# Optimization experiments

Measured on AMD Instinct MI355X. Metric: run time of the kernel, lower is better.

The kernel has to match this reference:

```python
import jax, jax.numpy as jnp
import numpy as np
import math

SIZE = 64
SCALE = math.sqrt(SIZE)
EPS = 1e-12  # torch F.normalize default eps

def l2_normalize(x, axis):
    n = jnp.linalg.norm(x, ord=2, axis=axis, keepdims=True)
    return x / jnp.maximum(n, EPS)

def setup_inputs() -> dict:
    key = jax.random.key(0)
    k1, k2, k3 = jax.random.split(key, 3)
    n, l, s, d, v = 8, 2048, 2048, SIZE, SIZE
    return {
        "query": jax.random.normal(k1, (n, l, d), dtype=jnp.float32),
        "key": jax.random.normal(k2, (n, s, d), dtype=jnp.float32),
        "value": jax.random.normal(k3, (n, s, v), dtype=jnp.float32),
        "mask": jnp.ones((n, l, s), dtype=bool),
    }

def reference(query, key, value, mask):
    # rank-3 query path with normalize=True (cosine attention)
    q = l2_normalize(query, 2)
    k = l2_normalize(key, 2)
    score = jnp.einsum('nlk,nsk->nls', q, k) / SCALE
    score = jnp.where(mask, score, -jnp.inf)
    score = jax.nn.softmax(score, axis=2)  # [n, l, s]
    # equivalent to (score.unsqueeze(3) * value.unsqueeze(1)).sum(2)
    output_value = jnp.einsum('nls,nsv->nlv', score, value)
    return (output_value, score)
```

## Files before the change

### kernel.cpp

```cpp
#include <hip/hip_runtime.h>
#include <hip/hip_bf16.h>
#include <math.h>


typedef __bf16 bf16x8 __attribute__((ext_vector_type(8)));
typedef __bf16 bf16x4 __attribute__((ext_vector_type(4)));
typedef float f32x4 __attribute__((ext_vector_type(4)));

#define NB 8
#define LL 2048
#define SS 2048
#define DD 64

__global__ __launch_bounds__(256) void prep_norm(const float* __restrict__ q,
                                                 const float* __restrict__ k,
                                                 __bf16* __restrict__ Qb,
                                                 __bf16* __restrict__ Kb) {
  int w = threadIdx.x >> 6, lane = threadIdx.x & 63;
  int r = blockIdx.x * 4 + w;
  const float* src;
  __bf16* dst;
  float extra;
  if (r < NB * LL) {
    src = q + (size_t)r * DD;
    dst = Qb + (size_t)r * DD;
    extra = 0.125f;
  } else {
    int rk = r - NB * LL;
    src = k + (size_t)rk * DD;
    dst = Kb + (size_t)rk * DD;
    extra = 1.0f;
  }
  float x = src[lane];
  float ss = x * x;
  ss += __shfl_xor(ss, 1);
  ss += __shfl_xor(ss, 2);
  ss += __shfl_xor(ss, 4);
  ss += __shfl_xor(ss, 8);
  ss += __shfl_xor(ss, 16);
  ss += __shfl_xor(ss, 32);
  float nrm = sqrtf(ss);
  float sc = extra / fmaxf(nrm, 1e-12f);
  dst[lane] = (__bf16)(x * sc);
}

__global__ __launch_bounds__(256) void prep_vt(const float* __restrict__ v,
                                               __bf16* __restrict__ Vt) {
  __shared__ __bf16 tile[64][72];
  int n = blockIdx.y;
  int s0 = blockIdx.x * 64;
  int t = threadIdx.x;
#pragma unroll
  for (int it = 0; it < 4; ++it) {
    int idx = t + it * 256;
    int s = idx >> 4, c = idx & 15;
    float4 f = *(const float4*)(v + ((size_t)(n * SS + s0 + s)) * DD + c * 4);
    tile[s][c * 4 + 0] = (__bf16)f.x;
    tile[s][c * 4 + 1] = (__bf16)f.y;
    tile[s][c * 4 + 2] = (__bf16)f.z;
    tile[s][c * 4 + 3] = (__bf16)f.w;
  }
  __syncthreads();
#pragma unroll
  for (int it = 0; it < 4; ++it) {
    int idx = t + it * 256;
    int vv = idx >> 4, c = idx & 15;
    bf16x4 o;
    o[0] = tile[c * 4 + 0][vv];
    o[1] = tile[c * 4 + 1][vv];
    o[2] = tile[c * 4 + 2][vv];
    o[3] = tile[c * 4 + 3][vv];
    *(bf16x4*)(Vt + ((size_t)(n * DD + vv)) * SS + s0 + c * 4) = o;
  }
}

__global__ __launch_bounds__(512, 4) void attn_main(const __bf16* __restrict__ Qb,
                                                    const __bf16* __restrict__ Kb,
                                                    const __bf16* __restrict__ Vt,
                                                    const int* __restrict__ mask,
                                                    float* __restrict__ out_val,
                                                    float* __restrict__ out_score) {
  __shared__ __bf16 e_lds[2][16][136];
  __shared__ float rs_lds[8][16];
  __shared__ float acc_red[4][16][17];

  const int n = blockIdx.y;
  const int l0 = blockIdx.x * 16;

  const int t = threadIdx.x;
  const int w = t >> 6;
  const int lane = t & 63;
  const int m16 = lane & 15;
  const int quad = lane >> 4;
  const int vg = w & 3;
  const int sh = (w >> 2) * 64;

  const __bf16* qrow = Qb + ((size_t)(n * LL + l0 + m16)) * DD;
  bf16x8 aq0 = *(const bf16x8*)(qrow + quad * 8);
  bf16x8 aq1 = *(const bf16x8*)(qrow + 32 + quad * 8);

  const __bf16* kbase = Kb + (size_t)n * SS * DD;
  const __bf16* vrow = Vt + ((size_t)(n * DD + vg * 16 + m16)) * SS + sh;
  const size_t mrow = ((size_t)(n * LL + l0 + m16)) * SS + w * 16 + quad * 4;
  const int* mptr = mask + mrow;

  f32x4 acc_o = {0.f, 0.f, 0.f, 0.f};
  float rsum = 0.f;
  bf16x4 stash[16];

  int4 mkb[4];
  mkb[0] = *(const int4*)(mptr + 0 * 128);
  mkb[1] = *(const int4*)(mptr + 1 * 128);
  mkb[2] = *(const int4*)(mptr + 2 * 128);
  mkb[3] = *(const int4*)(mptr + 3 * 128);

  bf16x8 kpa0, kpa1, kpb0, kpb1;
  {
    const __bf16* kr = kbase + (size_t)(w * 16 + m16) * DD;
    kpa0 = *(const bf16x8*)(kr + quad * 8);
    kpa1 = *(const bf16x8*)(kr + 32 + quad * 8);
  }

#pragma unroll
  for (int c = 0; c < 16; ++c) {
    const int sc = c * 128;
    bf16x8 bv0 = *(const bf16x8*)(vrow + sc + quad * 8);
    bf16x8 bv1 = *(const bf16x8*)(vrow + sc + 32 + quad * 8);
    const int4 mk = mkb[c & 3];
    if (c + 4 < 16) mkb[c & 3] = *(const int4*)(mptr + (size_t)(c + 4) * 128);
    if (c + 1 < 16) {
      const __bf16* kr = kbase + (size_t)(sc + 128 + w * 16 + m16) * DD;
      if (c & 1) {
        kpa0 = *(const bf16x8*)(kr + quad * 8);
        kpa1 = *(const bf16x8*)(kr + 32 + quad * 8);
      } else {
        kpb0 = *(const bf16x8*)(kr + quad * 8);
        kpb1 = *(const bf16x8*)(kr + 32 + quad * 8);
      }
    }
    const bf16x8 kb0 = (c & 1) ? kpb0 : kpa0;
    const bf16x8 kb1 = (c & 1) ? kpb1 : kpa1;
    f32x4 acc = {0.f, 0.f, 0.f, 0.f};
    acc = __builtin_amdgcn_mfma_f32_16x16x32_bf16(kb0, aq0, acc, 0, 0, 0);
    acc = __builtin_amdgcn_mfma_f32_16x16x32_bf16(kb1, aq1, acc, 0, 0, 0);
    float e0 = mk.x ? __expf(acc[0]) : 0.f;
    float e1 = mk.y ? __expf(acc[1]) : 0.f;
    float e2 = mk.z ? __expf(acc[2]) : 0.f;
    float e3 = mk.w ? __expf(acc[3]) : 0.f;
    rsum += (e0 + e1) + (e2 + e3);
    bf16x4 sv;
    sv[0] = (__bf16)e0;
    sv[1] = (__bf16)e1;
    sv[2] = (__bf16)e2;
    sv[3] = (__bf16)e3;
    stash[c] = sv;
    *(bf16x4*)(&e_lds[c & 1][m16][w * 16 + quad * 4]) = sv;
    asm volatile("s_waitcnt lgkmcnt(0)" ::: "memory");
    __builtin_amdgcn_s_barrier();
    bf16x8 ae0 = *(const bf16x8*)(&e_lds[c & 1][m16][sh + quad * 8]);
    bf16x8 ae1 = *(const bf16x8*)(&e_lds[c & 1][m16][sh + 32 + quad * 8]);
    acc_o = __builtin_amdgcn_mfma_f32_16x16x32_bf16(ae0, bv0, acc_o, 0, 0, 0);
    acc_o = __builtin_amdgcn_mfma_f32_16x16x32_bf16(ae1, bv1, acc_o, 0, 0, 0);
  }

  rsum += __shfl_xor(rsum, 16);
  rsum += __shfl_xor(rsum, 32);
  if (quad == 0) rs_lds[w][m16] = rsum;
  if (w >= 4) {
#pragma unroll
    for (int r = 0; r < 4; ++r) acc_red[vg][quad * 4 + r][m16] = acc_o[r];
  }
  __syncthreads();

  float tot = 0.f;
#pragma unroll
  for (int ww = 0; ww < 8; ++ww) tot += rs_lds[ww][m16];
  const float inv_s = 1.0f / tot;

  if (w < 4) {
#pragma unroll
    for (int r = 0; r < 4; ++r) {
      const int row = quad * 4 + r;
      float tr = 0.f;
#pragma unroll
      for (int ww = 0; ww < 8; ++ww) tr += rs_lds[ww][row];
      const float o = (acc_o[r] + acc_red[vg][row][m16]) / tr;
      out_val[((size_t)(n * LL + l0 + row)) * DD + vg * 16 + m16] = o;
    }
  }

  float* orow = out_score + mrow;
#pragma unroll
  for (int c = 0; c < 16; ++c) {
    float4 o;
    o.x = (float)stash[c][0] * inv_s;
    o.y = (float)stash[c][1] * inv_s;
    o.z = (float)stash[c][2] * inv_s;
    o.w = (float)stash[c][3] * inv_s;
    *(float4*)(orow + (size_t)c * 128) = o;
  }
}

extern "C" void kernel_launch(void* const* d_in, const int* in_sizes, int n_in,
                              void* d_out, int out_size, void* d_ws, size_t ws_size,
                              hipStream_t stream) {
  const float* q = (const float*)d_in[0];
  const float* k = (const float*)d_in[1];
  const float* v = (const float*)d_in[2];
  const int* mask = (const int*)d_in[3];

  float* out_val = (float*)d_out;
  float* out_score = out_val + (size_t)NB * LL * DD;

  __bf16* Qb = (__bf16*)d_ws;
  __bf16* Kb = Qb + (size_t)NB * LL * DD;
  __bf16* Vt = Kb + (size_t)NB * SS * DD;

  prep_norm<<<dim3((NB * LL * 2) / 4), dim3(256), 0, stream>>>(q, k, Qb, Kb);
  prep_vt<<<dim3(SS / 64, NB), dim3(256), 0, stream>>>(v, Vt);
  attn_main<<<dim3(LL / 16, NB), dim3(512), 0, stream>>>(Qb, Kb, Vt, mask, out_val, out_score);
}
```

Baseline: 294.6 us.

## Coalesce mask loads and score stores through LDS staging

Mask reads are re-mapped so each half-wavefront reads one contiguous 512-byte row segment. The mask is packed into byte flags in a double-buffered LDS array that the MFMA-layout lanes then read. Score output is staged through an LDS buffer in groups of four chunks, so each row's float4 stores are fully contiguous instead of scattered 16-byte pieces per lane. This aims to improve global coalescing of the two largest memory streams (the mask read and the score write), at the cost of extra LDS traffic, more shared memory and additional barriers.

```diff
diff --git a/kernel.cpp b/kernel.cpp
--- a/kernel.cpp
+++ b/kernel.cpp
@@ -81,8 +81,11 @@
                                                     float* __restrict__ out_val,
                                                     float* __restrict__ out_score) {
   __shared__ __bf16 e_lds[2][16][136];
+  __shared__ unsigned mb_lds[2][16][33];
   __shared__ float rs_lds[8][16];
   __shared__ float acc_red[4][16][17];
+  __shared__ float inv_row[16];
+  __shared__ __bf16 ep_buf[16][520];
 
   const int n = blockIdx.y;
   const int l0 = blockIdx.x * 16;
@@ -101,18 +104,18 @@
 
   const __bf16* kbase = Kb + (size_t)n * SS * DD;
   const __bf16* vrow = Vt + ((size_t)(n * DD + vg * 16 + m16)) * SS + sh;
-  const size_t mrow = ((size_t)(n * LL + l0 + m16)) * SS + w * 16 + quad * 4;
-  const int* mptr = mask + mrow;
+
+  const int mrow_st = t >> 5;
+  const int mcol_st = (t & 31) * 4;
+  const int* mgbase = mask + ((size_t)(n * LL + l0 + mrow_st)) * SS + mcol_st;
 
   f32x4 acc_o = {0.f, 0.f, 0.f, 0.f};
   float rsum = 0.f;
   bf16x4 stash[16];
 
-  int4 mkb[4];
-  mkb[0] = *(const int4*)(mptr + 0 * 128);
-  mkb[1] = *(const int4*)(mptr + 1 * 128);
-  mkb[2] = *(const int4*)(mptr + 2 * 128);
-  mkb[3] = *(const int4*)(mptr + 3 * 128);
+  int4 mreg[2];
+  mreg[0] = *(const int4*)(mgbase + 0 * 128);
+  mreg[1] = *(const int4*)(mgbase + 1 * 128);
 
   bf16x8 kpa0, kpa1, kpb0, kpb1;
   {
@@ -121,13 +124,19 @@
     kpa1 = *(const bf16x8*)(kr + 32 + quad * 8);
   }
 
+  {
+    const int4 m = mreg[0];
+    mb_lds[0][mrow_st][t & 31] = (unsigned)((m.x != 0) | ((m.y != 0) << 8) |
+                                            ((m.z != 0) << 16) | ((m.w != 0) << 24));
+  }
+  asm volatile("s_waitcnt lgkmcnt(0)" ::: "memory");
+  __builtin_amdgcn_s_barrier();
+
 #pragma unroll
   for (int c = 0; c < 16; ++c) {
     const int sc = c * 128;
     bf16x8 bv0 = *(const bf16x8*)(vrow + sc + quad * 8);
     bf16x8 bv1 = *(const bf16x8*)(vrow + sc + 32 + quad * 8);
-    const int4 mk = mkb[c & 3];
-    if (c + 4 < 16) mkb[c & 3] = *(const int4*)(mptr + (size_t)(c + 4) * 128);
     if (c + 1 < 16) {
       const __bf16* kr = kbase + (size_t)(sc + 128 + w * 16 + m16) * DD;
       if (c & 1) {
@@ -138,15 +147,23 @@
         kpb1 = *(const bf16x8*)(kr + 32 + quad * 8);
       }
     }
+    if (c + 2 < 16) mreg[c & 1] = *(const int4*)(mgbase + (size_t)(c + 2) * 128);
+    if (c + 1 < 16) {
+      const int4 m = mreg[(c + 1) & 1];
+      mb_lds[(c + 1) & 1][mrow_st][t & 31] =
+          (unsigned)((m.x != 0) | ((m.y != 0) << 8) | ((m.z != 0) << 16) |
+                     ((m.w != 0) << 24));
+    }
+    const unsigned mu = mb_lds[c & 1][m16][w * 4 + quad];
     const bf16x8 kb0 = (c & 1) ? kpb0 : kpa0;
     const bf16x8 kb1 = (c & 1) ? kpb1 : kpa1;
     f32x4 acc = {0.f, 0.f, 0.f, 0.f};
     acc = __builtin_amdgcn_mfma_f32_16x16x32_bf16(kb0, aq0, acc, 0, 0, 0);
     acc = __builtin_amdgcn_mfma_f32_16x16x32_bf16(kb1, aq1, acc, 0, 0, 0);
-    float e0 = mk.x ? __expf(acc[0]) : 0.f;
-    float e1 = mk.y ? __expf(acc[1]) : 0.f;
-    float e2 = mk.z ? __expf(acc[2]) : 0.f;
-    float e3 = mk.w ? __expf(acc[3]) : 0.f;
+    float e0 = (mu & 0x1u) ? __expf(acc[0]) : 0.f;
+    float e1 = (mu & 0x100u) ? __expf(acc[1]) : 0.f;
+    float e2 = (mu & 0x10000u) ? __expf(acc[2]) : 0.f;
+    float e3 = (mu & 0x1000000u) ? __expf(acc[3]) : 0.f;
     rsum += (e0 + e1) + (e2 + e3);
     bf16x4 sv;
     sv[0] = (__bf16)e0;
@@ -176,6 +193,7 @@
 #pragma unroll
   for (int ww = 0; ww < 8; ++ww) tot += rs_lds[ww][m16];
   const float inv_s = 1.0f / tot;
+  if (t < 16) inv_row[t] = inv_s;
 
   if (w < 4) {
 #pragma unroll
@@ -188,16 +206,32 @@
       out_val[((size_t)(n * LL + l0 + row)) * DD + vg * 16 + m16] = o;
     }
   }
-
-  float* orow = out_score + mrow;
-#pragma unroll
-  for (int c = 0; c < 16; ++c) {
-    float4 o;
-    o.x = (float)stash[c][0] * inv_s;
-    o.y = (float)stash[c][1] * inv_s;
-    o.z = (float)stash[c][2] * inv_s;
-    o.w = (float)stash[c][3] * inv_s;
-    *(float4*)(orow + (size_t)c * 128) = o;
+  __syncthreads();
+
+  const int erow = t >> 5;
+  const int ecol = (t & 31) * 4;
+  const float einv = inv_row[erow];
+  float* obase = out_score + ((size_t)(n * LL + l0 + erow)) * SS;
+#pragma unroll
+  for (int g = 0; g < 4; ++g) {
+#pragma unroll
+    for (int i = 0; i < 4; ++i) {
+      *(bf16x4*)(&ep_buf[m16][i * 128 + w * 16 + quad * 4]) = stash[g * 4 + i];
+    }
+    asm volatile("s_waitcnt lgkmcnt(0)" ::: "memory");
+    __builtin_amdgcn_s_barrier();
+#pragma unroll
+    for (int i = 0; i < 4; ++i) {
+      const bf16x4 ev = *(const bf16x4*)(&ep_buf[erow][ecol + i * 128]);
+      float4 o;
+      o.x = (float)ev[0] * einv;
+      o.y = (float)ev[1] * einv;
+      o.z = (float)ev[2] * einv;
+      o.w = (float)ev[3] * einv;
+      *(float4*)(obase + g * 512 + ecol + i * 128) = o;
+    }
+    asm volatile("s_waitcnt lgkmcnt(0)" ::: "memory");
+    __builtin_amdgcn_s_barrier();
   }
 }
 
```

Result: faster. 278.1 us (-5.6%).
